# Performance work log

Hardware: AMD Instinct MI355X
Metric: run time of the kernel (lower is better)

## Reference

```python
import jax, jax.numpy as jnp
import numpy as np

SRC_V, TGT_V = 30000, 32000
E, H, SRC_LEN, TGT_LEN, B = 256, 1024, 48, 48, 64


def _lstm_layer(x, h0, c0, W_ih, W_hh, b_ih, b_hh):
    """x: [T,B,in]; PyTorch gate order i,f,g,o. Returns (ys [T,B,H], h, c)."""
    b = b_ih + b_hh
    xg = jnp.einsum('tbi,gi->tbg', x, W_ih) + b  # precompute input gates for all steps
    def step(carry, xt):
        h, c = carry
        gates = xt + h @ W_hh.T
        i, f, g, o = jnp.split(gates, 4, axis=-1)
        c = jax.nn.sigmoid(f) * c + jax.nn.sigmoid(i) * jnp.tanh(g)
        h = jax.nn.sigmoid(o) * jnp.tanh(c)
        return (h, c), h
    (h, c), ys = jax.lax.scan(step, (h0, c0), xg)
    return ys, h, c


def setup_inputs() -> dict:
    key = jax.random.key(0)
    ks = jax.random.split(key, 24)
    s = 1.0 / np.sqrt(H)
    u = lambda k, shape: jax.random.uniform(k, shape, jnp.float32, -s, s)
    inp = {
        'source': jax.random.randint(ks[0], (SRC_LEN, B), 0, SRC_V),
        'target': jax.random.randint(ks[1], (TGT_LEN, B), 0, TGT_V),
        'enc_emb': jax.random.normal(ks[2], (SRC_V, E), jnp.float32) * 0.1,
        'dec_emb': jax.random.normal(ks[3], (TGT_V, E), jnp.float32) * 0.1,
        'fc_W': u(ks[4], (TGT_V, H)),
        'fc_b': u(ks[5], (TGT_V,)),
    }
    i = 6
    for pre, insz in (('e', E), ('d', E)):
        for l in range(2):
            in_l = insz if l == 0 else H
            inp[f'{pre}W_ih{l}'] = u(ks[i], (4 * H, in_l)); i += 1
            inp[f'{pre}W_hh{l}'] = u(ks[i], (4 * H, H)); i += 1
            inp[f'{pre}b_ih{l}'] = u(ks[i], (4 * H,)); i += 1
            inp[f'{pre}b_hh{l}'] = u(ks[i], (4 * H,)); i += 1
    return inp


def reference(source, target, enc_emb, dec_emb, fc_W, fc_b,
              eW_ih0, eW_hh0, eb_ih0, eb_hh0, eW_ih1, eW_hh1, eb_ih1, eb_hh1,
              dW_ih0, dW_hh0, db_ih0, db_hh0, dW_ih1, dW_hh1, db_ih1, db_hh1):
    T, Bsz = target.shape
    z = jnp.zeros((Bsz, H), jnp.float32)
    # encoder (dropout is identity at eval)
    xe = enc_emb[source]                                    # [S,B,E]
    y0, h0, c0 = _lstm_layer(xe, z, z, eW_ih0, eW_hh0, eb_ih0, eb_hh0)
    _, h1, c1 = _lstm_layer(y0, z, z, eW_ih1, eW_hh1, eb_ih1, eb_hh1)
    # decoder, fully teacher-forced: inputs target[0:T-1], fills outputs[1:]
    xd = dec_emb[target[:-1]]                               # [T-1,B,E]
    d0, _, _ = _lstm_layer(xd, h0, c0, dW_ih0, dW_hh0, db_ih0, db_hh0)
    d1, _, _ = _lstm_layer(d0, h1, c1, dW_ih1, dW_hh1, db_ih1, db_hh1)
    preds = jnp.einsum('tbh,vh->tbv', d1, fc_W) + fc_b      # [T-1,B,V]
    outputs = jnp.concatenate([jnp.zeros((1, Bsz, TGT_V), jnp.float32), preds], axis=0)
    return outputs
```

## Files before the change

kernel.cpp:

```cpp
#include <hip/hip_runtime.h>
#include <hip/hip_bf16.h>

#define H 1024
#define G4 4096
#define EDIM 256
#define BATCH 64
#define VOUT 32000

typedef __attribute__((ext_vector_type(8))) short bh8;
typedef __attribute__((ext_vector_type(4))) float f4;

__device__ __forceinline__ unsigned short f2bf(float f) {
  unsigned u = __float_as_uint(f);
  unsigned r = (u + 0x7fffu + ((u >> 16) & 1u)) >> 16;
  return (unsigned short)r;
}

__global__ void k_cvt(const float* __restrict__ s, unsigned short* __restrict__ d, int n8) {
  int i = blockIdx.x * 256 + threadIdx.x;
  if (i >= n8) return;
  const float4* sp = (const float4*)s;
  float4 a = sp[2 * (size_t)i];
  float4 b = sp[2 * (size_t)i + 1];
  bh8 o;
  o[0] = (short)f2bf(a.x); o[1] = (short)f2bf(a.y);
  o[2] = (short)f2bf(a.z); o[3] = (short)f2bf(a.w);
  o[4] = (short)f2bf(b.x); o[5] = (short)f2bf(b.y);
  o[6] = (short)f2bf(b.z); o[7] = (short)f2bf(b.w);
  *(bh8*)(d + 8 * (size_t)i) = o;
}

__global__ void k_bias(const float* __restrict__ bi, const float* __restrict__ bh,
                       float* __restrict__ out) {
  int i = blockIdx.x * 256 + threadIdx.x;
  out[i] = bi[i] + bh[i];
}

__global__ void k_zero(float4* __restrict__ p, int n4) {
  int i = blockIdx.x * 256 + threadIdx.x;
  if (i < n4) p[i] = make_float4(0.f, 0.f, 0.f, 0.f);
}

__global__ void k_gather(const int* __restrict__ idx, const float* __restrict__ emb,
                         unsigned short* __restrict__ out, int rows) {
  int t = blockIdx.x * 256 + threadIdx.x;
  int r = t >> 5, c8 = (t & 31) * 8;
  if (r >= rows) return;
  const float* e = emb + (size_t)idx[r] * EDIM + c8;
  bh8 o;
#pragma unroll
  for (int j = 0; j < 8; j++) o[j] = (short)f2bf(e[j]);
  *(bh8*)(out + (size_t)r * EDIM + c8) = o;
}

#define BM 128
#define BN 128
#define BKK 64
#define LDT 72

__launch_bounds__(256)
__global__ void k_gemm(const unsigned short* __restrict__ A, const unsigned short* __restrict__ B,
                       float* __restrict__ C, const float* __restrict__ bias,
                       int K, int ldc, int row_off, int m_valid) {
  __shared__ __align__(16) unsigned short As[BM * LDT];
  __shared__ __align__(16) unsigned short Bs[BM * LDT];
  int tm = blockIdx.y, tn = blockIdx.x;
  int tid = threadIdx.x;
  int lane = tid & 63, wv = tid >> 6;
  int wm = (wv >> 1) * 64, wn = (wv & 1) * 64;
  f4 acc[4][4] = {};
  const size_t a_base = (size_t)tm * BM * K;
  const size_t b_base = (size_t)tn * BN * K;
  for (int k0 = 0; k0 < K; k0 += BKK) {
#pragma unroll
    for (int i = 0; i < 4; i++) {
      int u = i * 256 + tid;
      int row = u >> 3;
      int ch = (u & 7) * 8;
      bh8 va = *(const bh8*)(A + a_base + (size_t)row * K + k0 + ch);
      bh8 vb = *(const bh8*)(B + b_base + (size_t)row * K + k0 + ch);
      *(bh8*)(As + row * LDT + ch) = va;
      *(bh8*)(Bs + row * LDT + ch) = vb;
    }
    __syncthreads();
#pragma unroll
    for (int kk = 0; kk < 2; kk++) {
      int ko = kk * 32 + (lane >> 4) * 8;
      bh8 af[4], bfr[4];
#pragma unroll
      for (int x = 0; x < 4; x++) {
        af[x]  = *(const bh8*)(As + (wm + x * 16 + (lane & 15)) * LDT + ko);
        bfr[x] = *(const bh8*)(Bs + (wn + x * 16 + (lane & 15)) * LDT + ko);
      }
#pragma unroll
      for (int mi = 0; mi < 4; mi++)
#pragma unroll
        for (int ni = 0; ni < 4; ni++)
          acc[mi][ni] = __builtin_amdgcn_mfma_f32_16x16x32_bf16(af[mi], bfr[ni], acc[mi][ni], 0, 0, 0);
    }
    __syncthreads();
  }
  int r0 = tm * BM + wm + (lane >> 4) * 4;
  int c0 = tn * BN + wn + (lane & 15);
#pragma unroll
  for (int mi = 0; mi < 4; mi++) {
#pragma unroll
    for (int ni = 0; ni < 4; ni++) {
      int col = c0 + ni * 16;
      float bv = bias ? bias[col] : 0.f;
#pragma unroll
      for (int j = 0; j < 4; j++) {
        int row = r0 + mi * 16 + j;
        if (row < m_valid)
          C[(size_t)(row_off + row) * ldc + col] = acc[mi][ni][j] + bv;
      }
    }
  }
}

struct Job {
  const float* xg;
  const unsigned short* hprev;
  unsigned short* hnext;
  float* c;
  const unsigned short* Whh;
  unsigned short* yout;
};
struct Job2 { Job j[2]; };

#define LDW 1032

__launch_bounds__(256)
__global__ void k_step(Job2 jobs) {
  __shared__ __align__(16) unsigned short Ws[32 * LDW];
  __shared__ float Gs[64 * 33];
  const Job& jb = jobs.j[blockIdx.x >> 7];
  int wg = blockIdx.x & 127;
  int tid = threadIdx.x, lane = tid & 63, wv = tid >> 6;

#pragma unroll
  for (int i = 0; i < 16; i++) {
    int u = i * 256 + tid;
    int row = u >> 7;
    int ch = (u & 127) * 8;
    int grow = ((row >> 3) << 10) + wg * 8 + (row & 7);
    bh8 v = *(const bh8*)(jb.Whh + (size_t)grow * H + ch);
    *(bh8*)(Ws + row * LDW + ch) = v;
  }
  __syncthreads();

  f4 acc0 = {}, acc1 = {};
  const unsigned short* hp = jb.hprev + (size_t)(wv * 16 + (lane & 15)) * H + (lane >> 4) * 8;
  const unsigned short* wp0 = Ws + (lane & 15) * LDW + (lane >> 4) * 8;
  const unsigned short* wp1 = Ws + (16 + (lane & 15)) * LDW + (lane >> 4) * 8;
#pragma unroll 8
  for (int kk = 0; kk < 32; kk++) {
    bh8 a  = *(const bh8*)(hp + kk * 32);
    bh8 b0 = *(const bh8*)(wp0 + kk * 32);
    bh8 b1 = *(const bh8*)(wp1 + kk * 32);
    acc0 = __builtin_amdgcn_mfma_f32_16x16x32_bf16(a, b0, acc0, 0, 0, 0);
    acc1 = __builtin_amdgcn_mfma_f32_16x16x32_bf16(a, b1, acc1, 0, 0, 0);
  }
#pragma unroll
  for (int j = 0; j < 4; j++) {
    int r = wv * 16 + (lane >> 4) * 4 + j;
    Gs[r * 33 + (lane & 15)]      = acc0[j];
    Gs[r * 33 + 16 + (lane & 15)] = acc1[j];
  }
  __syncthreads();

#pragma unroll
  for (int q = 0; q < 2; q++) {
    int idx = q * 256 + tid;
    int r = idx >> 3, hc = idx & 7;
    int gcb = wg * 8 + hc;
    float gi = Gs[r * 33 + hc]      + jb.xg[(size_t)r * G4 + gcb];
    float gf = Gs[r * 33 + 8 + hc]  + jb.xg[(size_t)r * G4 + 1024 + gcb];
    float gg = Gs[r * 33 + 16 + hc] + jb.xg[(size_t)r * G4 + 2048 + gcb];
    float go = Gs[r * 33 + 24 + hc] + jb.xg[(size_t)r * G4 + 3072 + gcb];
    float si = 1.f / (1.f + __expf(-gi));
    float sf = 1.f / (1.f + __expf(-gf));
    float so = 1.f / (1.f + __expf(-go));
    float tg = tanhf(gg);
    int ci = r * H + gcb;
    float cv = sf * jb.c[ci] + si * tg;
    float hv = so * tanhf(cv);
    jb.c[ci] = cv;
    unsigned short hb = f2bf(hv);
    jb.hnext[ci] = hb;
    if (jb.yout) jb.yout[ci] = hb;
  }
}

extern "C" void kernel_launch(void* const* d_in, const int* in_sizes, int n_in,
                              void* d_out, int out_size, void* d_ws, size_t ws_size,
                              hipStream_t stream) {
  const int*   src     = (const int*)d_in[0];
  const int*   tgt     = (const int*)d_in[1];
  const float* enc_emb = (const float*)d_in[2];
  const float* dec_emb = (const float*)d_in[3];
  const float* fc_W    = (const float*)d_in[4];
  const float* fc_b    = (const float*)d_in[5];
  const float* eW_ih0  = (const float*)d_in[6];
  const float* eW_hh0  = (const float*)d_in[7];
  const float* eb_ih0  = (const float*)d_in[8];
  const float* eb_hh0  = (const float*)d_in[9];
  const float* eW_ih1  = (const float*)d_in[10];
  const float* eW_hh1  = (const float*)d_in[11];
  const float* eb_ih1  = (const float*)d_in[12];
  const float* eb_hh1  = (const float*)d_in[13];
  const float* dW_ih0  = (const float*)d_in[14];
  const float* dW_hh0  = (const float*)d_in[15];
  const float* db_ih0  = (const float*)d_in[16];
  const float* db_hh0  = (const float*)d_in[17];
  const float* dW_ih1  = (const float*)d_in[18];
  const float* dW_hh1  = (const float*)d_in[19];
  const float* db_ih1  = (const float*)d_in[20];
  const float* db_hh1  = (const float*)d_in[21];

  char* p = (char*)d_ws;
  auto alloc = [&](size_t b) { char* r = p; p += (b + 255) & ~(size_t)255; return r; };

  char* zar = alloc(131072 * 2 + 262144 * 2);
  unsigned short* hbf_e0_0 = (unsigned short*)zar;
  unsigned short* hbf_e1_0 = (unsigned short*)(zar + 131072);
  float* c_e0 = (float*)(zar + 262144);
  float* c_e1 = (float*)(zar + 524288);
  unsigned short* hbf_e0_1 = (unsigned short*)alloc(131072);
  unsigned short* hbf_e1_1 = (unsigned short*)alloc(131072);
  unsigned short* hbf_d0[2] = {(unsigned short*)alloc(131072), (unsigned short*)alloc(131072)};
  unsigned short* hbf_d1[2] = {(unsigned short*)alloc(131072), (unsigned short*)alloc(131072)};

  unsigned short* w_eih0 = (unsigned short*)alloc((size_t)G4 * EDIM * 2);
  unsigned short* w_ehh0 = (unsigned short*)alloc((size_t)G4 * H * 2);
  unsigned short* w_eih1 = (unsigned short*)alloc((size_t)G4 * H * 2);
  unsigned short* w_ehh1 = (unsigned short*)alloc((size_t)G4 * H * 2);
  unsigned short* w_dih0 = (unsigned short*)alloc((size_t)G4 * EDIM * 2);
  unsigned short* w_dhh0 = (unsigned short*)alloc((size_t)G4 * H * 2);
  unsigned short* w_dih1 = (unsigned short*)alloc((size_t)G4 * H * 2);
  unsigned short* w_dhh1 = (unsigned short*)alloc((size_t)G4 * H * 2);
  unsigned short* w_fc   = (unsigned short*)alloc((size_t)VOUT * H * 2);

  unsigned short* xe  = (unsigned short*)alloc((size_t)3072 * EDIM * 2);
  unsigned short* xd  = (unsigned short*)alloc((size_t)3072 * EDIM * 2);
  unsigned short* y0  = (unsigned short*)alloc((size_t)3072 * H * 2);
  unsigned short* d0b = (unsigned short*)alloc((size_t)3072 * H * 2);
  unsigned short* d1b = (unsigned short*)alloc((size_t)3072 * H * 2);
  float* xgA = (float*)alloc((size_t)3072 * G4 * 4);
  float* xgB = (float*)alloc((size_t)3072 * G4 * 4);
  float* bias_e0 = (float*)alloc((size_t)4 * G4 * 4);
  float* bias_e1 = bias_e0 + G4;
  float* bias_d0 = bias_e0 + 2 * G4;
  float* bias_d1 = bias_e0 + 3 * G4;

  auto cvt = [&](const float* s, unsigned short* d, size_t n) {
    int n8 = (int)(n / 8);
    k_cvt<<<dim3((n8 + 255) / 256), dim3(256), 0, stream>>>(s, d, n8);
  };
  cvt(eW_ih0, w_eih0, (size_t)G4 * EDIM);
  cvt(eW_hh0, w_ehh0, (size_t)G4 * H);
  cvt(eW_ih1, w_eih1, (size_t)G4 * H);
  cvt(eW_hh1, w_ehh1, (size_t)G4 * H);
  cvt(dW_ih0, w_dih0, (size_t)G4 * EDIM);
  cvt(dW_hh0, w_dhh0, (size_t)G4 * H);
  cvt(dW_ih1, w_dih1, (size_t)G4 * H);
  cvt(dW_hh1, w_dhh1, (size_t)G4 * H);
  cvt(fc_W,   w_fc,   (size_t)VOUT * H);

  k_bias<<<dim3(16), dim3(256), 0, stream>>>(eb_ih0, eb_hh0, bias_e0);
  k_bias<<<dim3(16), dim3(256), 0, stream>>>(eb_ih1, eb_hh1, bias_e1);
  k_bias<<<dim3(16), dim3(256), 0, stream>>>(db_ih0, db_hh0, bias_d0);
  k_bias<<<dim3(16), dim3(256), 0, stream>>>(db_ih1, db_hh1, bias_d1);

  k_zero<<<dim3(192), dim3(256), 0, stream>>>((float4*)zar, 49152);
  k_zero<<<dim3(2000), dim3(256), 0, stream>>>((float4*)d_out, 512000);

  k_gather<<<dim3(384), dim3(256), 0, stream>>>(src, enc_emb, xe, 3072);
  k_gather<<<dim3(376), dim3(256), 0, stream>>>(tgt, dec_emb, xd, 3008);

  k_gemm<<<dim3(32, 24), dim3(256), 0, stream>>>(xe, w_eih0, xgA, bias_e0, EDIM, G4, 0, 3072);
  k_gemm<<<dim3(32, 24), dim3(256), 0, stream>>>(xd, w_dih0, xgB, bias_d0, EDIM, G4, 0, 3072);

  const size_t XGT = (size_t)BATCH * G4;
  const size_t HT  = (size_t)BATCH * H;

  for (int t = 0; t < 48; t++) {
    Job2 jj{};
    jj.j[0].xg = xgA + (size_t)t * XGT;
    jj.j[0].hprev = (t & 1) ? hbf_e0_1 : hbf_e0_0;
    jj.j[0].hnext = (t & 1) ? hbf_e0_0 : hbf_e0_1;
    jj.j[0].c = c_e0;
    jj.j[0].Whh = w_ehh0;
    jj.j[0].yout = y0 + (size_t)t * HT;
    k_step<<<dim3(128), dim3(256), 0, stream>>>(jj);
  }
  k_gemm<<<dim3(32, 24), dim3(256), 0, stream>>>(y0, w_eih1, xgA, bias_e1, H, G4, 0, 3072);

  for (int t = 0; t < 48; t++) {
    Job2 jj{};
    jj.j[0].xg = xgA + (size_t)t * XGT;
    jj.j[0].hprev = (t & 1) ? hbf_e1_1 : hbf_e1_0;
    jj.j[0].hnext = (t & 1) ? hbf_e1_0 : hbf_e1_1;
    jj.j[0].c = c_e1;
    jj.j[0].Whh = w_ehh1;
    jj.j[0].yout = nullptr;
    int nb = 128;
    if (t < 47) {
      jj.j[1].xg = xgB + (size_t)t * XGT;
      jj.j[1].hprev = (t == 0) ? hbf_e0_0 : hbf_d0[t & 1];
      jj.j[1].hnext = hbf_d0[(t + 1) & 1];
      jj.j[1].c = c_e0;
      jj.j[1].Whh = w_dhh0;
      jj.j[1].yout = d0b + (size_t)t * HT;
      nb = 256;
    }
    k_step<<<dim3(nb), dim3(256), 0, stream>>>(jj);
  }
  k_gemm<<<dim3(32, 24), dim3(256), 0, stream>>>(d0b, w_dih1, xgB, bias_d1, H, G4, 0, 3072);

  for (int t = 0; t < 47; t++) {
    Job2 jj{};
    jj.j[0].xg = xgB + (size_t)t * XGT;
    jj.j[0].hprev = (t == 0) ? hbf_e1_0 : hbf_d1[t & 1];
    jj.j[0].hnext = hbf_d1[(t + 1) & 1];
    jj.j[0].c = c_e1;
    jj.j[0].Whh = w_dhh1;
    jj.j[0].yout = d1b + (size_t)t * HT;
    k_step<<<dim3(128), dim3(256), 0, stream>>>(jj);
  }

  k_gemm<<<dim3(250, 24), dim3(256), 0, stream>>>(d1b, w_fc, (float*)d_out, fc_b, H, VOUT, 64, 3008);
}
```

Baseline: 2.648 ms.

## Fuse LSTM timesteps into persistent cooperative kernels; async LDS loads and XCD-aware GEMM tiles

```diff
diff --git a/kernel.cpp b/kernel.cpp
--- a/kernel.cpp
+++ b/kernel.cpp
@@ -6,6 +6,7 @@
 #define EDIM 256
 #define BATCH 64
 #define VOUT 32000
+#define LDW 1032
 
 typedef __attribute__((ext_vector_type(8))) short bh8;
 typedef __attribute__((ext_vector_type(4))) float f4;
@@ -14,6 +15,12 @@
   unsigned u = __float_as_uint(f);
   unsigned r = (u + 0x7fffu + ((u >> 16) & 1u)) >> 16;
   return (unsigned short)r;
+}
+
+__device__ __forceinline__ void gload16(const void* g, void* l) {
+  __builtin_amdgcn_global_load_lds(
+      (const __attribute__((address_space(1))) unsigned int*)g,
+      (__attribute__((address_space(3))) unsigned int*)l, 16, 0, 0);
 }
 
 __global__ void k_cvt(const float* __restrict__ s, unsigned short* __restrict__ d, int n8) {
@@ -53,55 +60,51 @@
   *(bh8*)(out + (size_t)r * EDIM + c8) = o;
 }
 
-#define BM 128
-#define BN 128
-#define BKK 64
-#define LDT 72
-
 __launch_bounds__(256)
 __global__ void k_gemm(const unsigned short* __restrict__ A, const unsigned short* __restrict__ B,
                        float* __restrict__ C, const float* __restrict__ bias,
-                       int K, int ldc, int row_off, int m_valid) {
-  __shared__ __align__(16) unsigned short As[BM * LDT];
-  __shared__ __align__(16) unsigned short Bs[BM * LDT];
-  int tm = blockIdx.y, tn = blockIdx.x;
-  int tid = threadIdx.x;
-  int lane = tid & 63, wv = tid >> 6;
-  int wm = (wv >> 1) * 64, wn = (wv & 1) * 64;
+                       int K, int ldc, int row_off, int m_valid, int grid_m) {
+  __shared__ __align__(16) unsigned short As[128 * 64];
+  __shared__ __align__(16) unsigned short Bs[128 * 64];
+  int nwg = gridDim.x, bid = blockIdx.x;
+  int q = nwg >> 3, r = nwg & 7;
+  int xcd = bid & 7, sub = bid >> 3;
+  int wg = ((xcd < r) ? xcd * (q + 1) : r * (q + 1) + (xcd - r) * q) + sub;
+  int tm = wg % grid_m, tn = wg / grid_m;
+  int tid = threadIdx.x, lane = tid & 63, wv = tid >> 6;
+  int wm = (wv >> 1) << 6, wn = (wv & 1) << 6;
   f4 acc[4][4] = {};
-  const size_t a_base = (size_t)tm * BM * K;
-  const size_t b_base = (size_t)tn * BN * K;
-  for (int k0 = 0; k0 < K; k0 += BKK) {
+  const size_t a_base = (size_t)tm * 128 * K;
+  const size_t b_base = (size_t)tn * 128 * K;
+  for (int k0 = 0; k0 < K; k0 += 64) {
 #pragma unroll
     for (int i = 0; i < 4; i++) {
-      int u = i * 256 + tid;
-      int row = u >> 3;
-      int ch = (u & 7) * 8;
-      bh8 va = *(const bh8*)(A + a_base + (size_t)row * K + k0 + ch);
-      bh8 vb = *(const bh8*)(B + b_base + (size_t)row * K + k0 + ch);
-      *(bh8*)(As + row * LDT + ch) = va;
-      *(bh8*)(Bs + row * LDT + ch) = vb;
+      int v = i * 256 + tid;
+      int row = v >> 3, ch = (v & 7) * 8;
+      int lbase = (v & ~63) * 8;
+      gload16(A + a_base + (size_t)row * K + k0 + ch, As + lbase);
+      gload16(B + b_base + (size_t)row * K + k0 + ch, Bs + lbase);
     }
     __syncthreads();
 #pragma unroll
     for (int kk = 0; kk < 2; kk++) {
       int ko = kk * 32 + (lane >> 4) * 8;
-      bh8 af[4], bfr[4];
+      bh8 af[4], bf[4];
 #pragma unroll
       for (int x = 0; x < 4; x++) {
-        af[x]  = *(const bh8*)(As + (wm + x * 16 + (lane & 15)) * LDT + ko);
-        bfr[x] = *(const bh8*)(Bs + (wn + x * 16 + (lane & 15)) * LDT + ko);
+        af[x] = *(const bh8*)(As + (wm + x * 16 + (lane & 15)) * 64 + ko);
+        bf[x] = *(const bh8*)(Bs + (wn + x * 16 + (lane & 15)) * 64 + ko);
       }
 #pragma unroll
       for (int mi = 0; mi < 4; mi++)
 #pragma unroll
         for (int ni = 0; ni < 4; ni++)
-          acc[mi][ni] = __builtin_amdgcn_mfma_f32_16x16x32_bf16(af[mi], bfr[ni], acc[mi][ni], 0, 0, 0);
+          acc[mi][ni] = __builtin_amdgcn_mfma_f32_16x16x32_bf16(af[mi], bf[ni], acc[mi][ni], 0, 0, 0);
     }
     __syncthreads();
   }
-  int r0 = tm * BM + wm + (lane >> 4) * 4;
-  int c0 = tn * BN + wn + (lane & 15);
+  int r0 = tm * 128 + wm + (lane >> 4) * 4;
+  int c0 = tn * 128 + wn + (lane & 15);
 #pragma unroll
   for (int mi = 0; mi < 4; mi++) {
 #pragma unroll
@@ -118,25 +121,25 @@
   }
 }
 
-struct Job {
+struct PhJob {
   const float* xg;
-  const unsigned short* hprev;
-  unsigned short* hnext;
+  const unsigned short* hinit;
+  unsigned short* hb0;
+  unsigned short* hb1;
   float* c;
   const unsigned short* Whh;
   unsigned short* yout;
+  int T;
 };
-struct Job2 { Job j[2]; };
-
-#define LDW 1032
-
-__launch_bounds__(256)
-__global__ void k_step(Job2 jobs) {
+struct PhArgs { PhJob j[2]; unsigned* ctr; int Tmax; };
+
+__global__ void __launch_bounds__(256, 1) k_phase(PhArgs a) {
   __shared__ __align__(16) unsigned short Ws[32 * LDW];
   __shared__ float Gs[64 * 33];
-  const Job& jb = jobs.j[blockIdx.x >> 7];
+  const PhJob jb = a.j[blockIdx.x >> 7];
   int wg = blockIdx.x & 127;
   int tid = threadIdx.x, lane = tid & 63, wv = tid >> 6;
+  unsigned nblk = gridDim.x;
 
 #pragma unroll
   for (int i = 0; i < 16; i++) {
@@ -144,51 +147,68 @@
     int row = u >> 7;
     int ch = (u & 127) * 8;
     int grow = ((row >> 3) << 10) + wg * 8 + (row & 7);
-    bh8 v = *(const bh8*)(jb.Whh + (size_t)grow * H + ch);
-    *(bh8*)(Ws + row * LDW + ch) = v;
+    *(bh8*)(Ws + row * LDW + ch) = *(const bh8*)(jb.Whh + (size_t)grow * H + ch);
   }
   __syncthreads();
 
-  f4 acc0 = {}, acc1 = {};
-  const unsigned short* hp = jb.hprev + (size_t)(wv * 16 + (lane & 15)) * H + (lane >> 4) * 8;
   const unsigned short* wp0 = Ws + (lane & 15) * LDW + (lane >> 4) * 8;
-  const unsigned short* wp1 = Ws + (16 + (lane & 15)) * LDW + (lane >> 4) * 8;
+  const unsigned short* wp1 = wp0 + 16 * LDW;
+
+  for (int t = 0; t < a.Tmax; t++) {
+    if (t < jb.T) {
+      const unsigned short* hprev = (t == 0) ? jb.hinit : ((t & 1) ? jb.hb1 : jb.hb0);
+      unsigned short* hnext = (t & 1) ? jb.hb0 : jb.hb1;
+      const float* xg = jb.xg + (size_t)t * (BATCH * G4);
+
+      f4 acc0 = {}, acc1 = {};
+      const unsigned short* hp = hprev + (size_t)(wv * 16 + (lane & 15)) * H + (lane >> 4) * 8;
 #pragma unroll 8
-  for (int kk = 0; kk < 32; kk++) {
-    bh8 a  = *(const bh8*)(hp + kk * 32);
-    bh8 b0 = *(const bh8*)(wp0 + kk * 32);
-    bh8 b1 = *(const bh8*)(wp1 + kk * 32);
-    acc0 = __builtin_amdgcn_mfma_f32_16x16x32_bf16(a, b0, acc0, 0, 0, 0);
-    acc1 = __builtin_amdgcn_mfma_f32_16x16x32_bf16(a, b1, acc1, 0, 0, 0);
-  }
-#pragma unroll
-  for (int j = 0; j < 4; j++) {
-    int r = wv * 16 + (lane >> 4) * 4 + j;
-    Gs[r * 33 + (lane & 15)]      = acc0[j];
-    Gs[r * 33 + 16 + (lane & 15)] = acc1[j];
-  }
-  __syncthreads();
-
-#pragma unroll
-  for (int q = 0; q < 2; q++) {
-    int idx = q * 256 + tid;
-    int r = idx >> 3, hc = idx & 7;
-    int gcb = wg * 8 + hc;
-    float gi = Gs[r * 33 + hc]      + jb.xg[(size_t)r * G4 + gcb];
-    float gf = Gs[r * 33 + 8 + hc]  + jb.xg[(size_t)r * G4 + 1024 + gcb];
-    float gg = Gs[r * 33 + 16 + hc] + jb.xg[(size_t)r * G4 + 2048 + gcb];
-    float go = Gs[r * 33 + 24 + hc] + jb.xg[(size_t)r * G4 + 3072 + gcb];
-    float si = 1.f / (1.f + __expf(-gi));
-    float sf = 1.f / (1.f + __expf(-gf));
-    float so = 1.f / (1.f + __expf(-go));
-    float tg = tanhf(gg);
-    int ci = r * H + gcb;
-    float cv = sf * jb.c[ci] + si * tg;
-    float hv = so * tanhf(cv);
-    jb.c[ci] = cv;
-    unsigned short hb = f2bf(hv);
-    jb.hnext[ci] = hb;
-    if (jb.yout) jb.yout[ci] = hb;
+      for (int kk = 0; kk < 32; kk++) {
+        bh8 av = *(const bh8*)(hp + kk * 32);
+        bh8 b0 = *(const bh8*)(wp0 + kk * 32);
+        bh8 b1 = *(const bh8*)(wp1 + kk * 32);
+        acc0 = __builtin_amdgcn_mfma_f32_16x16x32_bf16(av, b0, acc0, 0, 0, 0);
+        acc1 = __builtin_amdgcn_mfma_f32_16x16x32_bf16(av, b1, acc1, 0, 0, 0);
+      }
+#pragma unroll
+      for (int j = 0; j < 4; j++) {
+        int rr = wv * 16 + (lane >> 4) * 4 + j;
+        Gs[rr * 33 + (lane & 15)]      = acc0[j];
+        Gs[rr * 33 + 16 + (lane & 15)] = acc1[j];
+      }
+      __syncthreads();
+#pragma unroll
+      for (int qq = 0; qq < 2; qq++) {
+        int idx = qq * 256 + tid;
+        int rr = idx >> 3, hc = idx & 7;
+        int gcb = wg * 8 + hc;
+        float gi = Gs[rr * 33 + hc]      + xg[(size_t)rr * G4 + gcb];
+        float gf = Gs[rr * 33 + 8 + hc]  + xg[(size_t)rr * G4 + 1024 + gcb];
+        float gg = Gs[rr * 33 + 16 + hc] + xg[(size_t)rr * G4 + 2048 + gcb];
+        float go = Gs[rr * 33 + 24 + hc] + xg[(size_t)rr * G4 + 3072 + gcb];
+        float si = 1.f / (1.f + __expf(-gi));
+        float sf = 1.f / (1.f + __expf(-gf));
+        float so = 1.f / (1.f + __expf(-go));
+        float tg = tanhf(gg);
+        int ci = rr * H + gcb;
+        float cv = sf * jb.c[ci] + si * tg;
+        float hv = so * tanhf(cv);
+        jb.c[ci] = cv;
+        unsigned short hb = f2bf(hv);
+        hnext[ci] = hb;
+        if (jb.yout) jb.yout[(size_t)t * (BATCH * H) + ci] = hb;
+      }
+    }
+    __syncthreads();
+    if (tid == 0) {
+      __threadfence();
+      __hip_atomic_fetch_add(a.ctr, 1u, __ATOMIC_RELEASE, __HIP_MEMORY_SCOPE_AGENT);
+      unsigned tgt = (unsigned)(t + 1) * nblk;
+      while (__hip_atomic_load(a.ctr, __ATOMIC_ACQUIRE, __HIP_MEMORY_SCOPE_AGENT) < tgt)
+        __builtin_amdgcn_s_sleep(2);
+      __threadfence();
+    }
+    __syncthreads();
   }
 }
 
@@ -221,15 +241,20 @@
   char* p = (char*)d_ws;
   auto alloc = [&](size_t b) { char* r = p; p += (b + 255) & ~(size_t)255; return r; };
 
-  char* zar = alloc(131072 * 2 + 262144 * 2);
-  unsigned short* hbf_e0_0 = (unsigned short*)zar;
-  unsigned short* hbf_e1_0 = (unsigned short*)(zar + 131072);
-  float* c_e0 = (float*)(zar + 262144);
-  float* c_e1 = (float*)(zar + 524288);
+  char* zar = alloc(768 + 131072 * 2 + 262144 * 2);
+  unsigned* ctrA = (unsigned*)zar;
+  unsigned* ctrB = (unsigned*)(zar + 256);
+  unsigned* ctrC = (unsigned*)(zar + 512);
+  unsigned short* hbf_e0_0 = (unsigned short*)(zar + 768);
+  unsigned short* hbf_e1_0 = (unsigned short*)(zar + 768 + 131072);
+  float* c_e0 = (float*)(zar + 768 + 262144);
+  float* c_e1 = (float*)(zar + 768 + 524288);
   unsigned short* hbf_e0_1 = (unsigned short*)alloc(131072);
   unsigned short* hbf_e1_1 = (unsigned short*)alloc(131072);
-  unsigned short* hbf_d0[2] = {(unsigned short*)alloc(131072), (unsigned short*)alloc(131072)};
-  unsigned short* hbf_d1[2] = {(unsigned short*)alloc(131072), (unsigned short*)alloc(131072)};
+  unsigned short* hbf_d0_0 = (unsigned short*)alloc(131072);
+  unsigned short* hbf_d0_1 = (unsigned short*)alloc(131072);
+  unsigned short* hbf_d1_0 = (unsigned short*)alloc(131072);
+  unsigned short* hbf_d1_1 = (unsigned short*)alloc(131072);
 
   unsigned short* w_eih0 = (unsigned short*)alloc((size_t)G4 * EDIM * 2);
   unsigned short* w_ehh0 = (unsigned short*)alloc((size_t)G4 * H * 2);
@@ -272,62 +297,43 @@
   k_bias<<<dim3(16), dim3(256), 0, stream>>>(db_ih0, db_hh0, bias_d0);
   k_bias<<<dim3(16), dim3(256), 0, stream>>>(db_ih1, db_hh1, bias_d1);
 
-  k_zero<<<dim3(192), dim3(256), 0, stream>>>((float4*)zar, 49152);
+  k_zero<<<dim3(193), dim3(256), 0, stream>>>((float4*)zar, 49200);
   k_zero<<<dim3(2000), dim3(256), 0, stream>>>((float4*)d_out, 512000);
 
   k_gather<<<dim3(384), dim3(256), 0, stream>>>(src, enc_emb, xe, 3072);
   k_gather<<<dim3(376), dim3(256), 0, stream>>>(tgt, dec_emb, xd, 3008);
 
-  k_gemm<<<dim3(32, 24), dim3(256), 0, stream>>>(xe, w_eih0, xgA, bias_e0, EDIM, G4, 0, 3072);
-  k_gemm<<<dim3(32, 24), dim3(256), 0, stream>>>(xd, w_dih0, xgB, bias_d0, EDIM, G4, 0, 3072);
-
-  const size_t XGT = (size_t)BATCH * G4;
-  const size_t HT  = (size_t)BATCH * H;
-
-  for (int t = 0; t < 48; t++) {
-    Job2 jj{};
-    jj.j[0].xg = xgA + (size_t)t * XGT;
-    jj.j[0].hprev = (t & 1) ? hbf_e0_1 : hbf_e0_0;
-    jj.j[0].hnext = (t & 1) ? hbf_e0_0 : hbf_e0_1;
-    jj.j[0].c = c_e0;
-    jj.j[0].Whh = w_ehh0;
-    jj.j[0].yout = y0 + (size_t)t * HT;
-    k_step<<<dim3(128), dim3(256), 0, stream>>>(jj);
-  }
-  k_gemm<<<dim3(32, 24), dim3(256), 0, stream>>>(y0, w_eih1, xgA, bias_e1, H, G4, 0, 3072);
-
-  for (int t = 0; t < 48; t++) {
-    Job2 jj{};
-    jj.j[0].xg = xgA + (size_t)t * XGT;
-    jj.j[0].hprev = (t & 1) ? hbf_e1_1 : hbf_e1_0;
-    jj.j[0].hnext = (t & 1) ? hbf_e1_0 : hbf_e1_1;
-    jj.j[0].c = c_e1;
-    jj.j[0].Whh = w_ehh1;
-    jj.j[0].yout = nullptr;
-    int nb = 128;
-    if (t < 47) {
-      jj.j[1].xg = xgB + (size_t)t * XGT;
-      jj.j[1].hprev = (t == 0) ? hbf_e0_0 : hbf_d0[t & 1];
-      jj.j[1].hnext = hbf_d0[(t + 1) & 1];
-      jj.j[1].c = c_e0;
-      jj.j[1].Whh = w_dhh0;
-      jj.j[1].yout = d0b + (size_t)t * HT;
-      nb = 256;
-    }
-    k_step<<<dim3(nb), dim3(256), 0, stream>>>(jj);
-  }
-  k_gemm<<<dim3(32, 24), dim3(256), 0, stream>>>(d0b, w_dih1, xgB, bias_d1, H, G4, 0, 3072);
-
-  for (int t = 0; t < 47; t++) {
-    Job2 jj{};
-    jj.j[0].xg = xgB + (size_t)t * XGT;
-    jj.j[0].hprev = (t == 0) ? hbf_e1_0 : hbf_d1[t & 1];
-    jj.j[0].hnext = hbf_d1[(t + 1) & 1];
-    jj.j[0].c = c_e1;
-    jj.j[0].Whh = w_dhh1;
-    jj.j[0].yout = d1b + (size_t)t * HT;
-    k_step<<<dim3(128), dim3(256), 0, stream>>>(jj);
-  }
-
-  k_gemm<<<dim3(250, 24), dim3(256), 0, stream>>>(d1b, w_fc, (float*)d_out, fc_b, H, VOUT, 64, 3008);
-}
+  k_gemm<<<dim3(768), dim3(256), 0, stream>>>(xe, w_eih0, xgA, bias_e0, EDIM, G4, 0, 3072, 24);
+  k_gemm<<<dim3(768), dim3(256), 0, stream>>>(xd, w_dih0, xgB, bias_d0, EDIM, G4, 0, 3072, 24);
+
+  {
+    PhArgs pa{};
+    pa.j[0] = PhJob{xgA, hbf_e0_0, hbf_e0_0, hbf_e0_1, c_e0, w_ehh0, y0, 48};
+    pa.j[1] = pa.j[0];
+    pa.ctr = ctrA; pa.Tmax = 48;
+    void* args[] = {&pa};
+    hipLaunchCooperativeKernel((const void*)k_phase, dim3(128), dim3(256), args, 0, stream);
+  }
+  k_gemm<<<dim3(768), dim3(256), 0, stream>>>(y0, w_eih1, xgA, bias_e1, H, G4, 0, 3072, 24);
+
+  {
+    PhArgs pa{};
+    pa.j[0] = PhJob{xgA, hbf_e1_0, hbf_e1_0, hbf_e1_1, c_e1, w_ehh1, nullptr, 48};
+    pa.j[1] = PhJob{xgB, hbf_e0_0, hbf_d0_0, hbf_d0_1, c_e0, w_dhh0, d0b, 47};
+    pa.ctr = ctrB; pa.Tmax = 48;
+    void* args[] = {&pa};
+    hipLaunchCooperativeKernel((const void*)k_phase, dim3(256), dim3(256), args, 0, stream);
+  }
+  k_gemm<<<dim3(768), dim3(256), 0, stream>>>(d0b, w_dih1, xgB, bias_d1, H, G4, 0, 3072, 24);
+
+  {
+    PhArgs pa{};
+    pa.j[0] = PhJob{xgB, hbf_e1_0, hbf_d1_0, hbf_d1_1, c_e1, w_dhh1, d1b, 47};
+    pa.j[1] = pa.j[0];
+    pa.ctr = ctrC; pa.Tmax = 47;
+    void* args[] = {&pa};
+    hipLaunchCooperativeKernel((const void*)k_phase, dim3(128), dim3(256), args, 0, stream);
+  }
+
+  k_gemm<<<dim3(6000), dim3(256), 0, stream>>>(d1b, w_fc, (float*)d_out, fc_b, H, VOUT, 64, 3008, 24);
+}
```

Result: slower. 4.830 ms (+82.4%).
